# Kernel optimization log

Hardware: AMD Instinct MI355X
Metric: run time of the kernel (lower is better)

## Reference

```python
import jax, jax.numpy as jnp
import numpy as np

N_NODES = 100000
N_EDGES = 200000
D_LAT = 64
D_ENC = 32
N_FEAT = 2  # output features 'p', 'q'
D_IN = 2 * D_LAT + D_LAT + D_ENC + D_ENC  # 256
D_HID = 64


def setup_inputs() -> dict:
    key = jax.random.key(0)
    ks = jax.random.split(key, 12)
    return {
        "edge_array": jax.random.normal(ks[0], (N_EDGES, 4), dtype=jnp.float32),
        "h_local": jax.random.normal(ks[1], (N_NODES, D_LAT), dtype=jnp.float32),
        "h_global": jax.random.normal(ks[2], (1, D_LAT), dtype=jnp.float32),
        "enc_local": jax.random.normal(ks[3], (N_EDGES, D_ENC), dtype=jnp.float32),
        "enc_global": jax.random.normal(ks[4], (1, D_ENC), dtype=jnp.float32),
        "W1": jax.random.normal(ks[5], (N_FEAT, D_IN, D_HID), dtype=jnp.float32) / np.sqrt(D_IN),
        "b1": jnp.zeros((N_FEAT, D_HID), dtype=jnp.float32),
        "W2": jax.random.normal(ks[6], (N_FEAT, D_HID, D_HID), dtype=jnp.float32) / np.sqrt(D_HID),
        "b2": jnp.zeros((N_FEAT, D_HID), dtype=jnp.float32),
        "W3": jax.random.normal(ks[7], (N_FEAT, D_HID, 1), dtype=jnp.float32) / np.sqrt(D_HID),
        "b3": jnp.zeros((N_FEAT, 1), dtype=jnp.float32),
        "addr_from": jax.random.randint(ks[8], (N_EDGES,), 0, N_NODES, dtype=jnp.int32),
        "addr_to": jax.random.randint(ks[9], (N_EDGES,), 0, N_NODES, dtype=jnp.int32),
    }


def reference(edge_array, h_local, h_global, enc_local, enc_global,
              W1, b1, W2, b2, W3, b3, addr_from, addr_to):
    n = enc_local.shape[0]
    # gather node latents per address (drop/fill-0 semantics for out-of-range)
    g_from = h_local.at[addr_from].get(mode='fill', fill_value=0.0)  # [n, D_LAT]
    g_to = h_local.at[addr_to].get(mode='fill', fill_value=0.0)      # [n, D_LAT]
    # concat: [latents..., h_global*ones, enc_local, enc_global*ones]
    x = jnp.concatenate([
        g_from, g_to,
        jnp.broadcast_to(h_global, (n, h_global.shape[1])),
        enc_local,
        jnp.broadcast_to(enc_global, (n, enc_global.shape[1])),
    ], axis=1)  # [n, D_IN]
    # stacked per-feature MLPs (one MLP per output feature)
    h1 = jax.nn.leaky_relu(jnp.einsum('ni,fio->fno', x, W1) + b1[:, None, :])
    h2 = jax.nn.leaky_relu(jnp.einsum('fni,fio->fno', h1, W2) + b2[:, None, :])
    out = (jnp.einsum('fni,fio->fno', h2, W3) + b3[:, None, :])[..., 0]  # [F, n]
    isnan_mask = jnp.isnan(edge_array[:, 0])
    return jnp.where(isnan_mask[None, :], jnp.nan, out)
```

## Files before the change

### kernel.cpp

```cpp
#include <hip/hip_runtime.h>


#define OFF_W1 0
#define OFF_W2 40960
#define OFF_B1 57344
#define OFF_B2 57856
#define OFF_W3 58368
#define OFF_B3 58880
#define OFF_EA0 59392
#define H1_OFF 58944
#define NWAVE 8
#define LDS_TOTAL (H1_OFF + NWAVE * 2304)
#define PREP_W_BLOCKS 114

typedef __attribute__((ext_vector_type(8))) short bf16x8;
typedef __attribute__((ext_vector_type(4))) float f32x4;

__device__ inline short f2bf(float f) {
    unsigned u = __builtin_bit_cast(unsigned, f);
    u += 0x7FFFu + ((u >> 16) & 1u);
    return (short)(u >> 16);
}

__device__ inline float4 ld4(const float* p, bool v) {
    if (v) return *(const float4*)p;
    return make_float4(0.f, 0.f, 0.f, 0.f);
}

__device__ inline unsigned cvt_pk(float lo, float hi) {
    unsigned r;
    asm("v_cvt_pk_bf16_f32 %0, %1, %2" : "=v"(r) : "v"(lo), "v"(hi));
    return r;
}

__device__ inline bf16x8 pack8(float4 a, float4 b) {
    union { bf16x8 v; unsigned u[4]; } r;
    r.u[0] = cvt_pk(a.x, a.y);
    r.u[1] = cvt_pk(a.z, a.w);
    r.u[2] = cvt_pk(b.x, b.y);
    r.u[3] = cvt_pk(b.z, b.w);
    return r.v;
}

__global__ void prep_all(const float* __restrict__ W1, const float* __restrict__ b1,
                         const float* __restrict__ W2, const float* __restrict__ b2,
                         const float* __restrict__ W3, const float* __restrict__ b3,
                         const float* __restrict__ h_global, const float* __restrict__ enc_global,
                         const float* __restrict__ edge_array, const float* __restrict__ h_local,
                         int n_edges, int n8,
                         float* __restrict__ ea0, short* __restrict__ hbf,
                         char* __restrict__ ws) {
    int b = blockIdx.x;
    if (b >= PREP_W_BLOCKS) {
        int rb = b - PREP_W_BLOCKS;
        int eb = (n_edges + 255) >> 8;
        if (rb < eb) {
            int e = rb * 256 + threadIdx.x;
            if (e < n_edges) ea0[e] = ((const float4*)edge_array)[e].x;
        } else {
            int i = (rb - eb) * 256 + threadIdx.x;
            if (i < n8) {
                float4 a = ((const float4*)h_local)[2 * i];
                float4 c = ((const float4*)h_local)[2 * i + 1];
                ((bf16x8*)hbf)[i] = pack8(a, c);
            } else if (i < n8 + 8) {
                ((bf16x8*)hbf)[i] = (bf16x8){0, 0, 0, 0, 0, 0, 0, 0};
            }
        }
        return;
    }
    int idx = b * 256 + threadIdx.x;
    short* w1f = (short*)(ws + OFF_W1);
    short* w2f = (short*)(ws + OFF_W2);
    float* bp1 = (float*)(ws + OFF_B1);
    float* bp2 = (float*)(ws + OFF_B2);
    float* wp3 = (float*)(ws + OFF_W3);
    float* bp3 = (float*)(ws + OFF_B3);
    if (idx < 20480) {
        int f = idx / 10240, r0 = idx % 10240;
        int kk = r0 / 2048, r1 = r0 % 2048;
        int nn = r1 / 512,  r2 = r1 % 512;
        int l = r2 / 8,     j = r2 % 8;
        int kt = kk * 32 + (l >> 4) * 8 + j;
        int r = (kt < 128) ? kt : kt + 64;
        int c = nn * 16 + (l & 15);
        w1f[idx] = f2bf(W1[(f * 256 + r) * 64 + c]);
    } else if (idx < 28672) {
        int i2 = idx - 20480;
        int f = i2 / 4096, r0 = i2 % 4096;
        int kk = r0 / 2048, r1 = r0 % 2048;
        int nn = r1 / 512,  r2 = r1 % 512;
        int l = r2 / 8,     j = r2 % 8;
        int k = kk * 32 + (l >> 4) * 8 + j;
        int c = nn * 16 + (l & 15);
        w2f[i2] = f2bf(W2[(f * 64 + k) * 64 + c]);
    } else if (idx < 28800) {
        int i3 = idx - 28672; int f = i3 / 64, o = i3 % 64;
        float s = b1[f * 64 + o];
        for (int t = 0; t < 64; ++t) s += h_global[t] * W1[(f * 256 + 128 + t) * 64 + o];
        for (int t = 0; t < 32; ++t) s += enc_global[t] * W1[(f * 256 + 224 + t) * 64 + o];
        bp1[i3] = s;
    } else if (idx < 28928) {
        int i4 = idx - 28800; bp2[i4] = b2[i4];
    } else if (idx < 29056) {
        int i5 = idx - 28928; wp3[i5] = W3[i5];
    } else if (idx < 29058) {
        bp3[idx - 29056] = b3[idx - 29056];
    }
}

struct Tile { bf16x8 a0, a1, a2, a3; float4 e0, e1; float ea; };

template<bool HBF>
__device__ inline void gather_tile(int tbase, int n_edges, int n_nodes,
        const int* __restrict__ addr_from, const int* __restrict__ addr_to,
        const float* __restrict__ h_local, const short* __restrict__ hbf,
        const float* __restrict__ enc_local, const float* __restrict__ edge_array,
        const float* __restrict__ ea0, int col16, int g, Tile& T) {
    int e = tbase + col16;
    if (HBF) {
        int ec = e < n_edges ? e : n_edges - 1;
        int af = addr_from[ec], at = addr_to[ec];
        unsigned ra = (unsigned)af < (unsigned)n_nodes ? (unsigned)af : (unsigned)n_nodes;
        unsigned rt = (unsigned)at < (unsigned)n_nodes ? (unsigned)at : (unsigned)n_nodes;
        const short* pf = hbf + (size_t)ra * 64 + g * 8;
        const short* pt = hbf + (size_t)rt * 64 + g * 8;
        T.a0 = *(const bf16x8*)pf; T.a1 = *(const bf16x8*)(pf + 32);
        T.a2 = *(const bf16x8*)pt; T.a3 = *(const bf16x8*)(pt + 32);
        const float* pe = enc_local + (size_t)ec * 32 + g * 8;
        T.e0 = *(const float4*)pe; T.e1 = *(const float4*)(pe + 4);
        T.ea = ea0[ec];
    } else {
        bool ev = e < n_edges;
        int af = ev ? addr_from[e] : -1;
        int at = ev ? addr_to[e] : -1;
        bool afv = (unsigned)af < (unsigned)n_nodes;
        bool atv = (unsigned)at < (unsigned)n_nodes;
        const float* pf = h_local + (size_t)(afv ? af : 0) * 64 + g * 8;
        const float* pt = h_local + (size_t)(atv ? at : 0) * 64 + g * 8;
        T.a0 = pack8(ld4(pf, afv),      ld4(pf + 4, afv));
        T.a1 = pack8(ld4(pf + 32, afv), ld4(pf + 36, afv));
        T.a2 = pack8(ld4(pt, atv),      ld4(pt + 4, atv));
        T.a3 = pack8(ld4(pt + 32, atv), ld4(pt + 36, atv));
        const float* pe = enc_local + (size_t)(ev ? e : 0) * 32 + g * 8;
        T.e0 = ld4(pe, ev); T.e1 = ld4(pe + 4, ev);
        T.ea = ev ? edge_array[4 * e] : 0.f;
    }
}

template<bool HBF>
__global__ __launch_bounds__(512, 4) void main_kernel(
        const float* __restrict__ edge_array, const float* __restrict__ h_local,
        const float* __restrict__ enc_local,
        const int* __restrict__ addr_from, const int* __restrict__ addr_to,
        const char* __restrict__ ws, const float* __restrict__ ea0,
        const short* __restrict__ hbf, float* __restrict__ out,
        int n_edges, int n_nodes) {
    __shared__ __align__(16) char lds[LDS_TOTAL];
    const int tid = threadIdx.x;
    const int lane = tid & 63, wave = tid >> 6;
    const int col16 = lane & 15, g = lane >> 4;
    const int ntiles = (n_edges + 15) >> 4;
    const int wstride = gridDim.x * NWAVE;

    int t = blockIdx.x * NWAVE + wave;
    bool valid = t < ntiles;
    Tile cur;
    if (valid)
        gather_tile<HBF>(t * 16, n_edges, n_nodes, addr_from, addr_to, h_local,
                         hbf, enc_local, edge_array, ea0, col16, g, cur);

    #pragma unroll
    for (int it = 0; it < 7; ++it)
        ((float4*)lds)[it * 512 + tid] = ((const float4*)ws)[it * 512 + tid];
    if (tid < 100)
        ((float4*)(lds + 57344))[tid] = ((const float4*)(ws + 57344))[tid];
    __syncthreads();

    const float* bp1 = (const float*)(lds + OFF_B1);
    const float* bp2 = (const float*)(lds + OFF_B2);
    const float* wp3 = (const float*)(lds + OFF_W3);
    const float* bp3 = (const float*)(lds + OFF_B3);
    unsigned short* h1w = (unsigned short*)(lds + H1_OFF + wave * 2304);

    while (valid) {
        bf16x8 a1[5] = {cur.a0, cur.a1, cur.a2, cur.a3, pack8(cur.e0, cur.e1)};
        float ea = cur.ea;
        int tb = t * 16;

        int tn = t + wstride;
        bool vnext = tn < ntiles;
        if (vnext)
            gather_tile<HBF>(tn * 16, n_edges, n_nodes, addr_from, addr_to, h_local,
                             hbf, enc_local, edge_array, ea0, col16, g, cur);

        unsigned long long nanmask = __ballot(__builtin_isnan(ea));

        #pragma unroll
        for (int f = 0; f < 2; ++f) {
            f32x4 zero = {0.f, 0.f, 0.f, 0.f};
            f32x4 acc1[4] = {zero, zero, zero, zero};
            #pragma unroll
            for (int kk = 0; kk < 5; ++kk)
                #pragma unroll
                for (int nn = 0; nn < 4; ++nn) {
                    bf16x8 b = *(const bf16x8*)(lds + OFF_W1 + ((f * 5 + kk) * 4 + nn) * 1024 + lane * 16);
                    acc1[nn] = __builtin_amdgcn_mfma_f32_16x16x32_bf16(a1[kk], b, acc1[nn], 0, 0, 0);
                }

            #pragma unroll
            for (int nn = 0; nn < 4; ++nn) {
                float bv = bp1[f * 64 + col16 + 16 * nn];
                float v0 = acc1[nn][0] + bv, v1 = acc1[nn][1] + bv;
                float v2 = acc1[nn][2] + bv, v3 = acc1[nn][3] + bv;
                v0 = fmaxf(v0, 0.01f * v0); v1 = fmaxf(v1, 0.01f * v1);
                v2 = fmaxf(v2, 0.01f * v2); v3 = fmaxf(v3, 0.01f * v3);
                unsigned pk01 = cvt_pk(v0, v1), pk23 = cvt_pk(v2, v3);
                int base = g * 4 * 72 + col16 + 16 * nn;
                h1w[base]       = (unsigned short)pk01;
                h1w[base + 72]  = (unsigned short)(pk01 >> 16);
                h1w[base + 144] = (unsigned short)pk23;
                h1w[base + 216] = (unsigned short)(pk23 >> 16);
            }
            asm volatile("s_waitcnt lgkmcnt(0)" ::: "memory");

            bf16x8 a2[2];
            a2[0] = *(const bf16x8*)((const char*)h1w + col16 * 144 + g * 16);
            a2[1] = *(const bf16x8*)((const char*)h1w + col16 * 144 + 64 + g * 16);

            f32x4 acc2[4] = {zero, zero, zero, zero};
            #pragma unroll
            for (int kk = 0; kk < 2; ++kk)
                #pragma unroll
                for (int nn = 0; nn < 4; ++nn) {
                    bf16x8 b = *(const bf16x8*)(lds + OFF_W2 + ((f * 2 + kk) * 4 + nn) * 1024 + lane * 16);
                    acc2[nn] = __builtin_amdgcn_mfma_f32_16x16x32_bf16(a2[kk], b, acc2[nn], 0, 0, 0);
                }

            float p[4] = {0.f, 0.f, 0.f, 0.f};
            #pragma unroll
            for (int nn = 0; nn < 4; ++nn) {
                float b2v = bp2[f * 64 + col16 + 16 * nn];
                float w3v = wp3[f * 64 + col16 + 16 * nn];
                #pragma unroll
                for (int j = 0; j < 4; ++j) {
                    float h = acc2[nn][j] + b2v;
                    h = fmaxf(h, 0.01f * h);
                    p[j] += h * w3v;
                }
            }
            #pragma unroll
            for (int m = 1; m <= 8; m <<= 1) {
                #pragma unroll
                for (int j = 0; j < 4; ++j) p[j] += __shfl_xor(p[j], m, 64);
            }
            if (col16 == 0) {
                float b3v = bp3[f];
                #pragma unroll
                for (int j = 0; j < 4; ++j) {
                    int ee = tb + g * 4 + j;
                    if (ee < n_edges) {
                        float val = p[j] + b3v;
                        if ((nanmask >> (g * 4 + j)) & 1ull) val = __builtin_nanf("");
                        out[f * n_edges + ee] = val;
                    }
                }
            }
        }

        t = tn; valid = vnext;
    }
}

extern "C" void kernel_launch(void* const* d_in, const int* in_sizes, int n_in,
                              void* d_out, int out_size, void* d_ws, size_t ws_size,
                              hipStream_t stream) {
    const float* edge_array = (const float*)d_in[0];
    const float* h_local    = (const float*)d_in[1];
    const float* h_global   = (const float*)d_in[2];
    const float* enc_local  = (const float*)d_in[3];
    const float* enc_global = (const float*)d_in[4];
    const float* W1 = (const float*)d_in[5];
    const float* b1 = (const float*)d_in[6];
    const float* W2 = (const float*)d_in[7];
    const float* b2 = (const float*)d_in[8];
    const float* W3 = (const float*)d_in[9];
    const float* b3 = (const float*)d_in[10];
    const int* addr_from = (const int*)d_in[11];
    const int* addr_to   = (const int*)d_in[12];
    int n_edges = in_sizes[11];
    int n_nodes = in_sizes[1] / 64;
    int n8 = n_nodes * 8;
    char* ws = (char*)d_ws;

    size_t off_ea0 = OFF_EA0;
    size_t off_hbf = (off_ea0 + (size_t)n_edges * 4 + 255) & ~(size_t)255;
    size_t need = off_hbf + (size_t)(n_nodes + 1) * 128;
    bool use_hbf = ws_size >= need;
    float* ea0 = (float*)(ws + off_ea0);
    short* hbf = (short*)(ws + off_hbf);

    int eb = (n_edges + 255) / 256;
    int hb = (n8 + 8 + 255) / 256;
    int prep_blocks = PREP_W_BLOCKS + (use_hbf ? eb + hb : 0);
    hipLaunchKernelGGL(prep_all, dim3(prep_blocks), dim3(256), 0, stream,
                       W1, b1, W2, b2, W3, b3, h_global, enc_global,
                       edge_array, h_local, n_edges, n8, ea0, hbf, ws);

    int ntiles = (n_edges + 15) / 16;
    int nblk = 512;
    if (nblk * NWAVE > ntiles) nblk = (ntiles + NWAVE - 1) / NWAVE;
    if (use_hbf) {
        hipLaunchKernelGGL((main_kernel<true>), dim3(nblk), dim3(512), 0, stream,
                           edge_array, h_local, enc_local, addr_from, addr_to,
                           ws, ea0, hbf, (float*)d_out, n_edges, n_nodes);
    } else {
        hipLaunchKernelGGL((main_kernel<false>), dim3(nblk), dim3(512), 0, stream,
                           edge_array, h_local, enc_local, addr_from, addr_to,
                           ws, ea0, hbf, (float*)d_out, n_edges, n_nodes);
    }
}
```

Before: 39.39 us.

## Compute transposed MLP tiles so hidden activations stay in registers via shuffles

```diff
diff --git a/kernel.cpp b/kernel.cpp
--- a/kernel.cpp
+++ b/kernel.cpp
@@ -8,9 +8,8 @@
 #define OFF_W3 58368
 #define OFF_B3 58880
 #define OFF_EA0 59392
-#define H1_OFF 58944
 #define NWAVE 8
-#define LDS_TOTAL (H1_OFF + NWAVE * 2304)
+#define LDS_TOTAL 58944
 #define PREP_W_BLOCKS 114
 
 typedef __attribute__((ext_vector_type(8))) short bf16x8;
@@ -79,20 +78,20 @@
     if (idx < 20480) {
         int f = idx / 10240, r0 = idx % 10240;
         int kk = r0 / 2048, r1 = r0 % 2048;
-        int nn = r1 / 512,  r2 = r1 % 512;
+        int mm = r1 / 512,  r2 = r1 % 512;
         int l = r2 / 8,     j = r2 % 8;
         int kt = kk * 32 + (l >> 4) * 8 + j;
         int r = (kt < 128) ? kt : kt + 64;
-        int c = nn * 16 + (l & 15);
+        int c = mm * 16 + (l & 15);
         w1f[idx] = f2bf(W1[(f * 256 + r) * 64 + c]);
     } else if (idx < 28672) {
         int i2 = idx - 20480;
         int f = i2 / 4096, r0 = i2 % 4096;
         int kk = r0 / 2048, r1 = r0 % 2048;
-        int nn = r1 / 512,  r2 = r1 % 512;
+        int mm = r1 / 512,  r2 = r1 % 512;
         int l = r2 / 8,     j = r2 % 8;
         int k = kk * 32 + (l >> 4) * 8 + j;
-        int c = nn * 16 + (l & 15);
+        int c = mm * 16 + (l & 15);
         w2f[i2] = f2bf(W2[(f * 64 + k) * 64 + c]);
     } else if (idx < 28800) {
         int i3 = idx - 28672; int f = i3 / 64, o = i3 % 64;
@@ -160,6 +159,10 @@
     const int tid = threadIdx.x;
     const int lane = tid & 63, wave = tid >> 6;
     const int col16 = lane & 15, g = lane >> 4;
+    const int g4 = g * 4;
+    const bool hi = g >= 2;
+    const int srcA = col16 + 32 * (g & 1);
+    const int srcB = srcA + 16;
     const int ntiles = (n_edges + 15) >> 4;
     const int wstride = gridDim.x * NWAVE;
 
@@ -177,11 +180,8 @@
         ((float4*)(lds + 57344))[tid] = ((const float4*)(ws + 57344))[tid];
     __syncthreads();
 
-    const float* bp1 = (const float*)(lds + OFF_B1);
-    const float* bp2 = (const float*)(lds + OFF_B2);
-    const float* wp3 = (const float*)(lds + OFF_W3);
-    const float* bp3 = (const float*)(lds + OFF_B3);
-    unsigned short* h1w = (unsigned short*)(lds + H1_OFF + wave * 2304);
+    const float b3v0 = ((const float*)(lds + OFF_B3))[0];
+    const float b3v1 = ((const float*)(lds + OFF_B3))[1];
 
     while (valid) {
         bf16x8 a1[5] = {cur.a0, cur.a1, cur.a2, cur.a3, pack8(cur.e0, cur.e1)};
@@ -194,76 +194,78 @@
             gather_tile<HBF>(tn * 16, n_edges, n_nodes, addr_from, addr_to, h_local,
                              hbf, enc_local, edge_array, ea0, col16, g, cur);
 
-        unsigned long long nanmask = __ballot(__builtin_isnan(ea));
-
         #pragma unroll
         for (int f = 0; f < 2; ++f) {
-            f32x4 zero = {0.f, 0.f, 0.f, 0.f};
-            f32x4 acc1[4] = {zero, zero, zero, zero};
+            f32x4 acc1[4];
+            #pragma unroll
+            for (int mm = 0; mm < 4; ++mm)
+                acc1[mm] = *(const f32x4*)(lds + OFF_B1 + (f * 64 + mm * 16 + g4) * 4);
             #pragma unroll
             for (int kk = 0; kk < 5; ++kk)
                 #pragma unroll
-                for (int nn = 0; nn < 4; ++nn) {
-                    bf16x8 b = *(const bf16x8*)(lds + OFF_W1 + ((f * 5 + kk) * 4 + nn) * 1024 + lane * 16);
-                    acc1[nn] = __builtin_amdgcn_mfma_f32_16x16x32_bf16(a1[kk], b, acc1[nn], 0, 0, 0);
+                for (int mm = 0; mm < 4; ++mm) {
+                    bf16x8 w = *(const bf16x8*)(lds + OFF_W1 + ((f * 5 + kk) * 4 + mm) * 1024 + lane * 16);
+                    acc1[mm] = __builtin_amdgcn_mfma_f32_16x16x32_bf16(w, a1[kk], acc1[mm], 0, 0, 0);
                 }
 
-            #pragma unroll
-            for (int nn = 0; nn < 4; ++nn) {
-                float bv = bp1[f * 64 + col16 + 16 * nn];
-                float v0 = acc1[nn][0] + bv, v1 = acc1[nn][1] + bv;
-                float v2 = acc1[nn][2] + bv, v3 = acc1[nn][3] + bv;
+            unsigned pk[4][2];
+            #pragma unroll
+            for (int mm = 0; mm < 4; ++mm) {
+                float v0 = acc1[mm][0], v1 = acc1[mm][1];
+                float v2 = acc1[mm][2], v3 = acc1[mm][3];
                 v0 = fmaxf(v0, 0.01f * v0); v1 = fmaxf(v1, 0.01f * v1);
                 v2 = fmaxf(v2, 0.01f * v2); v3 = fmaxf(v3, 0.01f * v3);
-                unsigned pk01 = cvt_pk(v0, v1), pk23 = cvt_pk(v2, v3);
-                int base = g * 4 * 72 + col16 + 16 * nn;
-                h1w[base]       = (unsigned short)pk01;
-                h1w[base + 72]  = (unsigned short)(pk01 >> 16);
-                h1w[base + 144] = (unsigned short)pk23;
-                h1w[base + 216] = (unsigned short)(pk23 >> 16);
-            }
-            asm volatile("s_waitcnt lgkmcnt(0)" ::: "memory");
-
-            bf16x8 a2[2];
-            a2[0] = *(const bf16x8*)((const char*)h1w + col16 * 144 + g * 16);
-            a2[1] = *(const bf16x8*)((const char*)h1w + col16 * 144 + 64 + g * 16);
-
-            f32x4 acc2[4] = {zero, zero, zero, zero};
-            #pragma unroll
-            for (int kk = 0; kk < 2; ++kk)
+                pk[mm][0] = cvt_pk(v0, v1);
+                pk[mm][1] = cvt_pk(v2, v3);
+            }
+
+            f32x4 acc2[4];
+            #pragma unroll
+            for (int mm = 0; mm < 4; ++mm)
+                acc2[mm] = *(const f32x4*)(lds + OFF_B2 + (f * 64 + mm * 16 + g4) * 4);
+            #pragma unroll
+            for (int kk2 = 0; kk2 < 2; ++kk2) {
+                unsigned mL0 = pk[2 * kk2][0],     mL1 = pk[2 * kk2][1];
+                unsigned mH0 = pk[2 * kk2 + 1][0], mH1 = pk[2 * kk2 + 1][1];
+                unsigned t0L = (unsigned)__shfl((int)mL0, srcA, 64);
+                unsigned t0H = (unsigned)__shfl((int)mH0, srcA, 64);
+                unsigned t1L = (unsigned)__shfl((int)mL1, srcA, 64);
+                unsigned t1H = (unsigned)__shfl((int)mH1, srcA, 64);
+                unsigned t2L = (unsigned)__shfl((int)mL0, srcB, 64);
+                unsigned t2H = (unsigned)__shfl((int)mH0, srcB, 64);
+                unsigned t3L = (unsigned)__shfl((int)mL1, srcB, 64);
+                unsigned t3H = (unsigned)__shfl((int)mH1, srcB, 64);
+                union { bf16x8 v; unsigned u[4]; } bb;
+                bb.u[0] = hi ? t0H : t0L;
+                bb.u[1] = hi ? t1H : t1L;
+                bb.u[2] = hi ? t2H : t2L;
+                bb.u[3] = hi ? t3H : t3L;
                 #pragma unroll
-                for (int nn = 0; nn < 4; ++nn) {
-                    bf16x8 b = *(const bf16x8*)(lds + OFF_W2 + ((f * 2 + kk) * 4 + nn) * 1024 + lane * 16);
-                    acc2[nn] = __builtin_amdgcn_mfma_f32_16x16x32_bf16(a2[kk], b, acc2[nn], 0, 0, 0);
+                for (int mm = 0; mm < 4; ++mm) {
+                    bf16x8 w = *(const bf16x8*)(lds + OFF_W2 + ((f * 2 + kk2) * 4 + mm) * 1024 + lane * 16);
+                    acc2[mm] = __builtin_amdgcn_mfma_f32_16x16x32_bf16(w, bb.v, acc2[mm], 0, 0, 0);
                 }
-
-            float p[4] = {0.f, 0.f, 0.f, 0.f};
-            #pragma unroll
-            for (int nn = 0; nn < 4; ++nn) {
-                float b2v = bp2[f * 64 + col16 + 16 * nn];
-                float w3v = wp3[f * 64 + col16 + 16 * nn];
+            }
+
+            float p = 0.f;
+            #pragma unroll
+            for (int mm = 0; mm < 4; ++mm) {
+                f32x4 wv = *(const f32x4*)(lds + OFF_W3 + (f * 64 + mm * 16 + g4) * 4);
                 #pragma unroll
-                for (int j = 0; j < 4; ++j) {
-                    float h = acc2[nn][j] + b2v;
+                for (int jj = 0; jj < 4; ++jj) {
+                    float h = acc2[mm][jj];
                     h = fmaxf(h, 0.01f * h);
-                    p[j] += h * w3v;
+                    p = fmaf(h, wv[jj], p);
                 }
             }
-            #pragma unroll
-            for (int m = 1; m <= 8; m <<= 1) {
-                #pragma unroll
-                for (int j = 0; j < 4; ++j) p[j] += __shfl_xor(p[j], m, 64);
-            }
-            if (col16 == 0) {
-                float b3v = bp3[f];
-                #pragma unroll
-                for (int j = 0; j < 4; ++j) {
-                    int ee = tb + g * 4 + j;
-                    if (ee < n_edges) {
-                        float val = p[j] + b3v;
-                        if ((nanmask >> (g * 4 + j)) & 1ull) val = __builtin_nanf("");
-                        out[f * n_edges + ee] = val;
-                    }
+            p += __shfl_xor(p, 16, 64);
+            p += __shfl_xor(p, 32, 64);
+            if (lane < 16) {
+                int ee = tb + lane;
+                if (ee < n_edges) {
+                    float val = p + (f == 0 ? b3v0 : b3v1);
+                    if (__builtin_isnan(ea)) val = __builtin_nanf("");
+                    out[f * n_edges + ee] = val;
                 }
             }
         }
```

New measurement: 37.24 us. 1.06x faster.
